# Kernel tuning notes

Measured on AMD Instinct MI355X. Metric: run time of the kernel, lower is better.

## Reference

```python
import jax, jax.numpy as jnp
import numpy as np

E = 1024  # embed_dim
H = 16    # num_heads
D = E // H  # head_dim


def setup_inputs() -> dict:
    key = jax.random.key(0)
    ks = jax.random.split(key, 9)
    s = 0.02
    return {
        "hidden_state": jax.random.normal(ks[0], (4, 1024, E), jnp.float32),
        "Wq": jax.random.normal(ks[1], (H, D, E), jnp.float32) * s,
        "bq": jax.random.normal(ks[2], (H, D), jnp.float32) * s,
        "Wk": jax.random.normal(ks[3], (H, D, E), jnp.float32) * s,
        "bk": jax.random.normal(ks[4], (H, D), jnp.float32) * s,
        "Wv": jax.random.normal(ks[5], (H, D, E), jnp.float32) * s,
        "bv": jax.random.normal(ks[6], (H, D), jnp.float32) * s,
        "Wo": jax.random.normal(ks[7], (E, E), jnp.float32) * s,
        "bo": jax.random.normal(ks[8], (E,), jnp.float32) * s,
    }


def _mha(x, Wq, bq, Wk, bk, Wv, bv, Wo, bo):
    # Per-head linear projections (torch Linear: y = x W^T + b), batched over heads.
    q = jnp.einsum("bse,hde->bhsd", x, Wq) + bq[None, :, None, :]
    k = jnp.einsum("bse,hde->bhsd", x, Wk) + bk[None, :, None, :]
    v = jnp.einsum("bse,hde->bhsd", x, Wv) + bv[None, :, None, :]
    scores = jnp.einsum("bhsd,bhtd->bhst", q, k) / jnp.sqrt(jnp.asarray(D, x.dtype))
    w = jax.nn.softmax(scores, axis=-1)  # F.softmax default -> last dim
    o = jnp.einsum("bhst,bhtd->bhsd", w, v)
    # concat heads along last dim: [B,S,H*D] in head order (matches torch.cat)
    B, _, S, _ = o.shape
    o = jnp.transpose(o, (0, 2, 1, 3)).reshape(B, S, H * D)
    return o @ Wo.T + bo


def reference(hidden_state, Wq, bq, Wk, bk, Wv, bv, Wo, bo):
    return _mha(hidden_state, Wq, bq, Wk, bk, Wv, bv, Wo, bo)
```

## Files before the change

### kernel.cpp

```cpp
#include <hip/hip_runtime.h>
#include <hip/hip_bf16.h>
#include <stdint.h>

#define E_DIM 1024
#define H_NUM 16
#define D_DIM 64
#define B_NUM 4
#define S_LEN 1024

typedef __attribute__((ext_vector_type(8))) short bf16x8;
typedef __attribute__((ext_vector_type(4))) short bf16x4;
typedef __attribute__((ext_vector_type(4))) float f32x4;

#define SOFTMAX_C2 0.18033688011112042f

__device__ inline ushort f2b(float x) {
    __hip_bfloat16 h = __float2bfloat16(x);
    return *(ushort*)&h;
}
__device__ inline float b2f(ushort u) {
    __hip_bfloat16 h = *(__hip_bfloat16*)&u;
    return __bfloat162float(h);
}
__device__ inline uint pk2(float a, float b) {
    __hip_bfloat162 h = __float22bfloat162_rn(make_float2(a, b));
    return *(uint*)&h;
}

__device__ inline void gld16(const ushort* g, ushort* l) {
    __builtin_amdgcn_global_load_lds((const __attribute__((address_space(1))) void*)g,
                                     (__attribute__((address_space(3))) void*)l, 16, 0, 0);
}

__global__ __launch_bounds__(256)
void convert_all(const float* __restrict__ X,  const float* __restrict__ Wq,
                 const float* __restrict__ Wk, const float* __restrict__ Wv,
                 const float* __restrict__ Wo,
                 ushort* __restrict__ Xb, ushort* __restrict__ Wcat,
                 ushort* __restrict__ Wob)
{
    const int bid = blockIdx.x;
    const float* src; ushort* dst; size_t off;
    if (bid < 4096)      { src = X;  dst = Xb;   off = (size_t)bid * 1024; }
    else if (bid < 5120) { src = Wq; dst = Wcat;              off = (size_t)(bid - 4096) * 1024; }
    else if (bid < 6144) { src = Wk; dst = Wcat + (1u << 20); off = (size_t)(bid - 5120) * 1024; }
    else if (bid < 7168) { src = Wv; dst = Wcat + (2u << 20); off = (size_t)(bid - 6144) * 1024; }
    else                 { src = Wo; dst = Wob;               off = (size_t)(bid - 7168) * 1024; }
    const size_t i = off + (size_t)threadIdx.x * 4;
    float4 v = *(const float4*)&src[i];
    ushort4 o;
    o.x = f2b(v.x); o.y = f2b(v.y); o.z = f2b(v.z); o.w = f2b(v.w);
    *(ushort4*)&dst[i] = o;
}

__global__ __launch_bounds__(256, 3)
void gemm_qkv(const ushort* __restrict__ A, const ushort* __restrict__ Bw,
              const float* __restrict__ b0, const float* __restrict__ b1,
              const float* __restrict__ b2,
              ushort* __restrict__ Qb, ushort* __restrict__ Kb,
              ushort* __restrict__ Vt_g, int K)
{
    __shared__ __align__(16) ushort SM[24576];
    ushort* As = SM;
    ushort* Bs = SM + 16384;

    const int tid  = threadIdx.x;
    const int wave = tid >> 6;
    const int lane = tid & 63;
    const int quad = lane >> 4;
    const int l16  = lane & 15;
    const int wm   = wave & 1;
    const int wn   = wave >> 1;
    const int m0   = blockIdx.x * 128;
    const int n0   = blockIdx.y * 64;

    f32x4 acc[4][2] = {};

    auto stageA = [&](int buf, int k0) {
#pragma unroll
        for (int i = 0; i < 4; ++i) {
            const int e   = i * 256 + tid;
            const int row = e >> 3;
            const int gc8 = ((e & 7) ^ (row & 7)) * 8;
            gld16(&A[(size_t)(m0 + row) * K + k0 + gc8], &As[buf * 8192 + e * 8]);
        }
    };
    auto stageB = [&](int buf, int k0) {
#pragma unroll
        for (int i = 0; i < 2; ++i) {
            const int e   = i * 256 + tid;
            const int row = e >> 3;
            const int gc8 = ((e & 7) ^ (row & 7)) * 8;
            gld16(&Bw[(size_t)(n0 + row) * K + k0 + gc8], &Bs[buf * 4096 + e * 8]);
        }
    };

    stageA(0, 0); stageB(0, 0);
    __syncthreads();

    const int nk = K >> 6;
    const int xa = (l16 & 7) * 8;
    for (int ki = 0; ki < nk; ++ki) {
        const int cur = ki & 1;
        if (ki + 1 < nk) { stageA(cur ^ 1, (ki + 1) << 6); stageB(cur ^ 1, (ki + 1) << 6); }

#pragma unroll
        for (int ks = 0; ks < 2; ++ks) {
            const int lc = (ks * 32 + quad * 8) ^ xa;
            bf16x8 af[4], bf[2];
#pragma unroll
            for (int mi = 0; mi < 4; ++mi)
                af[mi] = *(const bf16x8*)&As[cur * 8192 + (wm * 64 + mi * 16 + l16) * 64 + lc];
#pragma unroll
            for (int ni = 0; ni < 2; ++ni)
                bf[ni] = *(const bf16x8*)&Bs[cur * 4096 + (wn * 32 + ni * 16 + l16) * 64 + lc];
#pragma unroll
            for (int mi = 0; mi < 4; ++mi)
#pragma unroll
                for (int ni = 0; ni < 2; ++ni)
                    acc[mi][ni] = __builtin_amdgcn_mfma_f32_16x16x32_bf16(af[mi], bf[ni], acc[mi][ni], 0, 0, 0);
        }
        __syncthreads();
    }

    const int seg   = n0 >> 10;
    const int cbase = n0 & 1023;
    const float* bp = (seg == 0) ? b0 : (seg == 1) ? b1 : b2;
    const float scl = (seg == 0) ? SOFTMAX_C2 : 1.0f;

    if (seg < 2) {
        ushort* T = SM;
#pragma unroll
        for (int ni = 0; ni < 2; ++ni) {
            const int nloc = wn * 32 + ni * 16 + l16;
            const float bv = bp[cbase + nloc];
#pragma unroll
            for (int mi = 0; mi < 4; ++mi)
#pragma unroll
                for (int r = 0; r < 4; ++r)
                    T[(wm * 64 + mi * 16 + quad * 4 + r) * 72 + nloc] =
                        f2b((acc[mi][ni][r] + bv) * scl);
        }
        __syncthreads();
        ushort* dst = (seg == 0) ? Qb : Kb;
        const int row = tid >> 1, half = tid & 1;
        const ushort* s = &T[row * 72 + half * 32];
        ushort* d = &dst[(size_t)(m0 + row) * 1024 + cbase + half * 32];
#pragma unroll
        for (int j = 0; j < 4; ++j)
            *(uint4*)(d + j * 8) = *(const uint4*)(s + j * 8);
    } else {
        ushort* Tt = SM;
        const int hh = cbase >> 6;
        const int b  = m0 >> 10, sbase = m0 & 1023;
#pragma unroll
        for (int ni = 0; ni < 2; ++ni) {
            const int nloc = wn * 32 + ni * 16 + l16;
            const float bv = bp[cbase + nloc];
#pragma unroll
            for (int mi = 0; mi < 4; ++mi) {
                const int mloc = wm * 64 + mi * 16 + quad * 4;
                ushort4 pk;
                pk.x = f2b(acc[mi][ni][0] + bv);
                pk.y = f2b(acc[mi][ni][1] + bv);
                pk.z = f2b(acc[mi][ni][2] + bv);
                pk.w = f2b(acc[mi][ni][3] + bv);
                *(ushort4*)&Tt[nloc * 136 + mloc] = pk;
            }
        }
        __syncthreads();
        const int nrow = tid >> 2, qtr = tid & 3;
        const ushort* s = &Tt[nrow * 136 + qtr * 32];
        ushort* d = &Vt_g[(((size_t)(b * 16 + hh)) * 64 + nrow) * 1024 + sbase + qtr * 32];
#pragma unroll
        for (int j = 0; j < 4; ++j)
            *(uint4*)(d + j * 8) = *(const uint4*)(s + j * 8);
    }
}

__global__ __launch_bounds__(256, 8)
void attention7(const ushort* __restrict__ Qg, const ushort* __restrict__ Kg,
                const ushort* __restrict__ Vg,
                ushort* __restrict__ Opart, float* __restrict__ Lpart)
{
    __shared__ __align__(16) ushort SM[9216];

    const int tid  = threadIdx.x;
    const int w    = tid >> 6;
    const int lane = tid & 63;
    const int quad = lane >> 4;
    const int l16  = lane & 15;

    const int gid = blockIdx.x;
    const int qt  = (gid >> 3) & 15;
    const int grp = (gid & 7) | ((gid >> 7) << 3);
    const int bh  = grp & 63;
    const int th  = grp >> 6;
    const int b   = bh >> 4;
    const int h   = bh & 15;
    const size_t tbase = ((size_t)b * S_LEN) * E_DIM + (size_t)h * D_DIM;
    const size_t vbase = (size_t)bh * D_DIM * S_LEN;
    const int t0 = th * 512;

    const ushort* qrow = Qg + tbase + (size_t)(qt * 64 + w * 16 + l16) * E_DIM + quad * 8;
    bf16x8 qf[2];
    qf[0] = *(const bf16x8*)qrow;
    qf[1] = *(const bf16x8*)(qrow + 32);

    const int krow = tid >> 3, kslot = tid & 7;
    const int vr   = tid >> 2, vc = (tid & 3) * 8;

    auto stageK = [&](int buf, int tg) {
        gld16(&Kg[tbase + (size_t)(tg + krow) * E_DIM + ((kslot ^ (krow & 7)) * 8)],
              &SM[buf * 2048 + tid * 8]);
    };

    stageK(0, t0);
    {
        uint4 v0 = *(const uint4*)&Vg[vbase + (size_t)vr * S_LEN + t0 + vc];
        *(uint4*)&SM[4096 + vr * 40 + vc] = v0;
    }
    __syncthreads();

    float lq = 0.0f;
    f32x4 oacc[4] = {};
    const int xk = (l16 & 7);

    for (int kt = 0; kt < 16; ++kt) {
        const int cur = kt & 1;

        uint4 vpre;
        if (kt < 15) {
            const int tg = t0 + (kt + 1) * 32;
            stageK(cur ^ 1, tg);
            vpre = *(const uint4*)&Vg[vbase + (size_t)vr * S_LEN + tg + vc];
        }

        f32x4 sacc[2] = {};
#pragma unroll
        for (int mt = 0; mt < 2; ++mt)
#pragma unroll
            for (int ks = 0; ks < 2; ++ks) {
                bf16x8 kf = *(const bf16x8*)&SM[cur * 2048 + (mt * 16 + l16) * 64 +
                                                (((ks * 4 + quad) ^ xk) * 8)];
                sacc[mt] = __builtin_amdgcn_mfma_f32_16x16x32_bf16(kf, qf[ks], sacc[mt], 0, 0, 0);
            }

        bf16x4 pf[2];
        float rs = 0.0f;
#pragma unroll
        for (int mt = 0; mt < 2; ++mt) {
            float p0 = exp2f(sacc[mt][0]);
            float p1 = exp2f(sacc[mt][1]);
            float p2 = exp2f(sacc[mt][2]);
            float p3 = exp2f(sacc[mt][3]);
            rs += (p0 + p1) + (p2 + p3);
            union { uint uu[2]; bf16x4 v; } pk;
            pk.uu[0] = pk2(p0, p1);
            pk.uu[1] = pk2(p2, p3);
            pf[mt] = pk.v;
        }
        lq += rs;

#pragma unroll
        for (int nb = 0; nb < 4; ++nb)
#pragma unroll
            for (int kb = 0; kb < 2; ++kb) {
                bf16x4 vf = *(const bf16x4*)&SM[4096 + cur * 2560 +
                                                (nb * 16 + l16) * 40 + kb * 16 + quad * 4];
                oacc[nb] = __builtin_amdgcn_mfma_f32_16x16x16bf16_1k(pf[kb], vf, oacc[nb], 0, 0, 0);
            }

        if (kt < 15)
            *(uint4*)&SM[4096 + (cur ^ 1) * 2560 + vr * 40 + vc] = vpre;
        __syncthreads();
    }

    lq += __shfl_xor(lq, 16);
    lq += __shfl_xor(lq, 32);
    const size_t obase = ((size_t)(th * 64 + bh)) * S_LEN;
    if (lane < 16)
        Lpart[obase + qt * 64 + w * 16 + l16] = lq;

    ushort* T = SM;
#pragma unroll
    for (int nb = 0; nb < 4; ++nb)
#pragma unroll
        for (int r = 0; r < 4; ++r)
            T[(w * 16 + quad * 4 + r) * 72 + nb * 16 + l16] = f2b(oacc[nb][r]);
    __syncthreads();
    {
        const int row = tid >> 2, c16 = (tid & 3) * 16;
        const ushort* s = &T[row * 72 + c16];
        ushort* d = &Opart[(obase + qt * 64 + row) * 64 + c16];
        *(uint4*)(d)     = *(const uint4*)(s);
        *(uint4*)(d + 8) = *(const uint4*)(s + 8);
    }
}

__global__ __launch_bounds__(256, 4)
void gemm_out(const ushort* __restrict__ Opart, const float* __restrict__ Lpart,
              const ushort* __restrict__ Bw, const float* __restrict__ bias,
              float* __restrict__ Cout)
{
    __shared__ __align__(16) ushort SM[17408];
    ushort* As = SM;
    ushort* Bs = SM + 9216;

    const int tid  = threadIdx.x;
    const int w    = tid >> 6;
    const int lane = tid & 63;
    const int quad = lane >> 4;
    const int l16  = lane & 15;
    const int m0   = blockIdx.x * 64;
    const int n0   = blockIdx.y * 64;

    const int arow = tid >> 2;
    const int acol = (tid & 3) * 16;
    const int m    = m0 + arow;
    const int ab   = m >> 10;
    const int as   = m & 1023;

    f32x4 acc[4] = {};

    auto loadA = [&](int ki, uint4* o0, uint4* o1, float* linv) {
        const int bh = ab * 16 + ki;
        const size_t p0 = ((size_t)bh * 1024 + as) * 64 + acol;
        const size_t p1 = ((size_t)(64 + bh) * 1024 + as) * 64 + acol;
#pragma unroll
        for (int j = 0; j < 2; ++j) {
            o0[j] = *(const uint4*)&Opart[p0 + j * 8];
            o1[j] = *(const uint4*)&Opart[p1 + j * 8];
        }
        const float l0 = Lpart[(size_t)bh * 1024 + as];
        const float l1 = Lpart[(size_t)(64 + bh) * 1024 + as];
        *linv = 1.0f / (l0 + l1);
    };
    auto writeA = [&](int buf, const uint4* o0, const uint4* o1, float linv) {
        ushort* dst = &As[buf * 4608 + arow * 72 + acol];
#pragma unroll
        for (int j = 0; j < 2; ++j) {
            const ushort* a = (const ushort*)&o0[j];
            const ushort* c = (const ushort*)&o1[j];
            union { uint uu[4]; uint4 v; } pk;
            pk.uu[0] = pk2((b2f(a[0]) + b2f(c[0])) * linv, (b2f(a[1]) + b2f(c[1])) * linv);
            pk.uu[1] = pk2((b2f(a[2]) + b2f(c[2])) * linv, (b2f(a[3]) + b2f(c[3])) * linv);
            pk.uu[2] = pk2((b2f(a[4]) + b2f(c[4])) * linv, (b2f(a[5]) + b2f(c[5])) * linv);
            pk.uu[3] = pk2((b2f(a[6]) + b2f(c[6])) * linv, (b2f(a[7]) + b2f(c[7])) * linv);
            *(uint4*)(dst + j * 8) = pk.v;
        }
    };
    auto stageB = [&](int buf, int k0) {
#pragma unroll
        for (int i = 0; i < 2; ++i) {
            const int e   = i * 256 + tid;
            const int row = e >> 3;
            const int gc8 = ((e & 7) ^ (row & 7)) * 8;
            gld16(&Bw[(size_t)(n0 + row) * 1024 + k0 + gc8], &Bs[buf * 4096 + e * 8]);
        }
    };

    {
        uint4 o0[2], o1[2]; float linv;
        loadA(0, o0, o1, &linv);
        writeA(0, o0, o1, linv);
        stageB(0, 0);
    }
    __syncthreads();

    const int xa = (l16 & 7) * 8;
    for (int ki = 0; ki < 16; ++ki) {
        const int cur = ki & 1;

        uint4 o0[2], o1[2]; float linv;
        if (ki + 1 < 16) {
            loadA(ki + 1, o0, o1, &linv);
            stageB(cur ^ 1, (ki + 1) << 6);
        }

#pragma unroll
        for (int ks = 0; ks < 2; ++ks) {
            bf16x8 af = *(const bf16x8*)&As[cur * 4608 + (w * 16 + l16) * 72 + ks * 32 + quad * 8];
#pragma unroll
            for (int nb = 0; nb < 4; ++nb) {
                const int lcB = (ks * 32 + quad * 8) ^ xa;
                bf16x8 bf = *(const bf16x8*)&Bs[cur * 4096 + (nb * 16 + l16) * 64 + lcB];
                acc[nb] = __builtin_amdgcn_mfma_f32_16x16x32_bf16(af, bf, acc[nb], 0, 0, 0);
            }
        }

        if (ki + 1 < 16) writeA(cur ^ 1, o0, o1, linv);
        __syncthreads();
    }

    float* Tf = (float*)SM;
#pragma unroll
    for (int nb = 0; nb < 4; ++nb) {
        const float bv = bias[n0 + nb * 16 + l16];
#pragma unroll
        for (int r = 0; r < 4; ++r)
            Tf[(w * 16 + quad * 4 + r) * 68 + nb * 16 + l16] = acc[nb][r] + bv;
    }
    __syncthreads();
    {
        const int row = tid >> 2, c16 = (tid & 3) * 16;
        const float* s = &Tf[row * 68 + c16];
        float* d = &Cout[(size_t)(m0 + row) * 1024 + n0 + c16];
#pragma unroll
        for (int j = 0; j < 4; ++j)
            *(float4*)(d + j * 4) = *(const float4*)(s + j * 4);
    }
}

extern "C" void kernel_launch(void* const* d_in, const int* in_sizes, int n_in,
                              void* d_out, int out_size, void* d_ws, size_t ws_size,
                              hipStream_t stream)
{
    (void)in_sizes; (void)n_in; (void)out_size; (void)ws_size;

    const float* X  = (const float*)d_in[0];
    const float* Wq = (const float*)d_in[1];
    const float* bq = (const float*)d_in[2];
    const float* Wk = (const float*)d_in[3];
    const float* bk = (const float*)d_in[4];
    const float* Wv = (const float*)d_in[5];
    const float* bv = (const float*)d_in[6];
    const float* Wo = (const float*)d_in[7];
    const float* bo = (const float*)d_in[8];

    const size_t MEG = 1u << 20;
    ushort* ws    = (ushort*)d_ws;
    ushort* Xb    = ws;
    ushort* Wcat  = ws + 4 * MEG;
    ushort* Wob   = ws + 7 * MEG;
    ushort* Qb    = ws + 8 * MEG;
    ushort* Kb    = ws + 12 * MEG;
    ushort* Vtg   = ws + 16 * MEG;
    ushort* Opart = ws + 20 * MEG;
    float*  Lpart = (float*)(ws + 28 * MEG);

    dim3 blk(256);

    convert_all<<<8192, blk, 0, stream>>>(X, Wq, Wk, Wv, Wo, Xb, Wcat, Wob);

    gemm_qkv<<<dim3(32, 48), blk, 0, stream>>>(Xb, Wcat, bq, bk, bv,
                                               Qb, Kb, Vtg, E_DIM);

    attention7<<<2048, blk, 0, stream>>>(Qb, Kb, Vtg, Opart, Lpart);

    gemm_out<<<dim3(64, 16), blk, 0, stream>>>(Opart, Lpart, Wob, bo,
                                               (float*)d_out);
}
```

Before: 188.5 us.

## Process two query sub-tiles per warp to reuse K/V fragments

Each attention block now covers 128 query rows instead of 64, with every wave handling two 16-row sub-tiles. Each K and V fragment loaded from shared memory then feeds two MFMAs, which halves LDS and global K/V traffic per query row and halves the grid to 1024 blocks. The V staging row pitch also changes from 40 to 36 elements. In exchange, register pressure roughly doubles for accumulators, launch bounds drop to 4 blocks per CU, and the smaller grid gives fewer blocks to spread across CUs.

```diff
diff --git a/kernel.cpp b/kernel.cpp
--- a/kernel.cpp
+++ b/kernel.cpp
@@ -178,8 +178,8 @@
     }
 }
 
-__global__ __launch_bounds__(256, 8)
-void attention7(const ushort* __restrict__ Qg, const ushort* __restrict__ Kg,
+__global__ __launch_bounds__(256, 4)
+void attention8(const ushort* __restrict__ Qg, const ushort* __restrict__ Kg,
                 const ushort* __restrict__ Vg,
                 ushort* __restrict__ Opart, float* __restrict__ Lpart)
 {
@@ -192,8 +192,8 @@
     const int l16  = lane & 15;
 
     const int gid = blockIdx.x;
-    const int qt  = (gid >> 3) & 15;
-    const int grp = (gid & 7) | ((gid >> 7) << 3);
+    const int qt  = (gid >> 3) & 7;
+    const int grp = (gid & 7) | ((gid >> 6) << 3);
     const int bh  = grp & 63;
     const int th  = grp >> 6;
     const int b   = bh >> 4;
@@ -202,10 +202,14 @@
     const size_t vbase = (size_t)bh * D_DIM * S_LEN;
     const int t0 = th * 512;
 
-    const ushort* qrow = Qg + tbase + (size_t)(qt * 64 + w * 16 + l16) * E_DIM + quad * 8;
-    bf16x8 qf[2];
-    qf[0] = *(const bf16x8*)qrow;
-    qf[1] = *(const bf16x8*)(qrow + 32);
+    bf16x8 qf[2][2];
+#pragma unroll
+    for (int i = 0; i < 2; ++i) {
+        const ushort* qrow = Qg + tbase +
+            (size_t)(qt * 128 + w * 32 + i * 16 + l16) * E_DIM + quad * 8;
+        qf[i][0] = *(const bf16x8*)qrow;
+        qf[i][1] = *(const bf16x8*)(qrow + 32);
+    }
 
     const int krow = tid >> 3, kslot = tid & 7;
     const int vr   = tid >> 2, vc = (tid & 3) * 8;
@@ -218,12 +222,12 @@
     stageK(0, t0);
     {
         uint4 v0 = *(const uint4*)&Vg[vbase + (size_t)vr * S_LEN + t0 + vc];
-        *(uint4*)&SM[4096 + vr * 40 + vc] = v0;
+        *(uint4*)&SM[4096 + vr * 36 + vc] = v0;
     }
     __syncthreads();
 
-    float lq = 0.0f;
-    f32x4 oacc[4] = {};
+    float lq[2] = {0.0f, 0.0f};
+    f32x4 oacc[2][4] = {};
     const int xk = (l16 & 7);
 
     for (int kt = 0; kt < 16; ++kt) {
@@ -236,65 +240,83 @@
             vpre = *(const uint4*)&Vg[vbase + (size_t)vr * S_LEN + tg + vc];
         }
 
-        f32x4 sacc[2] = {};
+        f32x4 sacc[2][2] = {};
 #pragma unroll
         for (int mt = 0; mt < 2; ++mt)
 #pragma unroll
             for (int ks = 0; ks < 2; ++ks) {
                 bf16x8 kf = *(const bf16x8*)&SM[cur * 2048 + (mt * 16 + l16) * 64 +
                                                 (((ks * 4 + quad) ^ xk) * 8)];
-                sacc[mt] = __builtin_amdgcn_mfma_f32_16x16x32_bf16(kf, qf[ks], sacc[mt], 0, 0, 0);
+#pragma unroll
+                for (int i = 0; i < 2; ++i)
+                    sacc[i][mt] = __builtin_amdgcn_mfma_f32_16x16x32_bf16(
+                        kf, qf[i][ks], sacc[i][mt], 0, 0, 0);
             }
 
-        bf16x4 pf[2];
-        float rs = 0.0f;
-#pragma unroll
-        for (int mt = 0; mt < 2; ++mt) {
-            float p0 = exp2f(sacc[mt][0]);
-            float p1 = exp2f(sacc[mt][1]);
-            float p2 = exp2f(sacc[mt][2]);
-            float p3 = exp2f(sacc[mt][3]);
-            rs += (p0 + p1) + (p2 + p3);
-            union { uint uu[2]; bf16x4 v; } pk;
-            pk.uu[0] = pk2(p0, p1);
-            pk.uu[1] = pk2(p2, p3);
-            pf[mt] = pk.v;
-        }
-        lq += rs;
+        bf16x4 pf[2][2];
+#pragma unroll
+        for (int i = 0; i < 2; ++i) {
+            float rs = 0.0f;
+#pragma unroll
+            for (int mt = 0; mt < 2; ++mt) {
+                float p0 = exp2f(sacc[i][mt][0]);
+                float p1 = exp2f(sacc[i][mt][1]);
+                float p2 = exp2f(sacc[i][mt][2]);
+                float p3 = exp2f(sacc[i][mt][3]);
+                rs += (p0 + p1) + (p2 + p3);
+                union { uint uu[2]; bf16x4 v; } pk;
+                pk.uu[0] = pk2(p0, p1);
+                pk.uu[1] = pk2(p2, p3);
+                pf[i][mt] = pk.v;
+            }
+            lq[i] += rs;
+        }
 
 #pragma unroll
         for (int nb = 0; nb < 4; ++nb)
 #pragma unroll
             for (int kb = 0; kb < 2; ++kb) {
-                bf16x4 vf = *(const bf16x4*)&SM[4096 + cur * 2560 +
-                                                (nb * 16 + l16) * 40 + kb * 16 + quad * 4];
-                oacc[nb] = __builtin_amdgcn_mfma_f32_16x16x16bf16_1k(pf[kb], vf, oacc[nb], 0, 0, 0);
+                bf16x4 vf = *(const bf16x4*)&SM[4096 + cur * 2304 +
+                                                (nb * 16 + l16) * 36 + kb * 16 + quad * 4];
+#pragma unroll
+                for (int i = 0; i < 2; ++i)
+                    oacc[i][nb] = __builtin_amdgcn_mfma_f32_16x16x16bf16_1k(
+                        pf[i][kb], vf, oacc[i][nb], 0, 0, 0);
             }
 
         if (kt < 15)
-            *(uint4*)&SM[4096 + (cur ^ 1) * 2560 + vr * 40 + vc] = vpre;
+            *(uint4*)&SM[4096 + (cur ^ 1) * 2304 + vr * 36 + vc] = vpre;
         __syncthreads();
     }
 
-    lq += __shfl_xor(lq, 16);
-    lq += __shfl_xor(lq, 32);
     const size_t obase = ((size_t)(th * 64 + bh)) * S_LEN;
-    if (lane < 16)
-        Lpart[obase + qt * 64 + w * 16 + l16] = lq;
+#pragma unroll
+    for (int i = 0; i < 2; ++i) {
+        lq[i] += __shfl_xor(lq[i], 16);
+        lq[i] += __shfl_xor(lq[i], 32);
+    }
+    if (lane < 16) {
+        Lpart[obase + qt * 128 + w * 32 + l16]      = lq[0];
+        Lpart[obase + qt * 128 + w * 32 + 16 + l16] = lq[1];
+    }
 
     ushort* T = SM;
 #pragma unroll
-    for (int nb = 0; nb < 4; ++nb)
-#pragma unroll
-        for (int r = 0; r < 4; ++r)
-            T[(w * 16 + quad * 4 + r) * 72 + nb * 16 + l16] = f2b(oacc[nb][r]);
+    for (int i = 0; i < 2; ++i)
+#pragma unroll
+        for (int nb = 0; nb < 4; ++nb)
+#pragma unroll
+            for (int r = 0; r < 4; ++r)
+                T[(w * 32 + i * 16 + quad * 4 + r) * 72 + nb * 16 + l16] =
+                    f2b(oacc[i][nb][r]);
     __syncthreads();
     {
-        const int row = tid >> 2, c16 = (tid & 3) * 16;
-        const ushort* s = &T[row * 72 + c16];
-        ushort* d = &Opart[(obase + qt * 64 + row) * 64 + c16];
-        *(uint4*)(d)     = *(const uint4*)(s);
-        *(uint4*)(d + 8) = *(const uint4*)(s + 8);
+        const int row = tid >> 1, half = tid & 1;
+        const ushort* s = &T[row * 72 + half * 32];
+        ushort* d = &Opart[(obase + qt * 128 + row) * 64 + half * 32];
+#pragma unroll
+        for (int j = 0; j < 4; ++j)
+            *(uint4*)(d + j * 8) = *(const uint4*)(s + j * 8);
     }
 }
 
@@ -446,7 +468,7 @@
     gemm_qkv<<<dim3(32, 48), blk, 0, stream>>>(Xb, Wcat, bq, bk, bv,
                                                Qb, Kb, Vtg, E_DIM);
 
-    attention7<<<2048, blk, 0, stream>>>(Qb, Kb, Vtg, Opart, Lpart);
+    attention8<<<1024, blk, 0, stream>>>(Qb, Kb, Vtg, Opart, Lpart);
 
     gemm_out<<<dim3(64, 16), blk, 0, stream>>>(Opart, Lpart, Wob, bo,
                                                (float*)d_out);
```

Result: no change. 186.8 us (-0.9%).

## Drop key-split in attention, normalize in-kernel, and stream normalized output to GEMM

Applied to the files above, without the earlier changes.

Attention no longer splits the key range into two halves with partial outputs and row sums. Each block now processes all 1024 keys, normalizes by the reciprocal row sum, and writes bf16 output directly in [B,S,E] layout. The output projection can then stage A straight into LDS with async global-to-LDS copies, dropping the combine/rescale step and the partial-sum buffers. This halves the attention grid to 1024 blocks, each with a longer loop, which lowers parallelism. It also swaps exp2f for the raw hardware exp2 intrinsic and shrinks the V tile padding.

```diff
diff --git a/kernel.cpp b/kernel.cpp
--- a/kernel.cpp
+++ b/kernel.cpp
@@ -26,6 +26,7 @@
     __hip_bfloat162 h = __float22bfloat162_rn(make_float2(a, b));
     return *(uint*)&h;
 }
+__device__ inline float fexp2(float x) { return __builtin_amdgcn_exp2f(x); }
 
 __device__ inline void gld16(const ushort* g, ushort* l) {
     __builtin_amdgcn_global_load_lds((const __attribute__((address_space(1))) void*)g,
@@ -179,9 +180,8 @@
 }
 
 __global__ __launch_bounds__(256, 8)
-void attention7(const ushort* __restrict__ Qg, const ushort* __restrict__ Kg,
-                const ushort* __restrict__ Vg,
-                ushort* __restrict__ Opart, float* __restrict__ Lpart)
+void attention11(const ushort* __restrict__ Qg, const ushort* __restrict__ Kg,
+                 const ushort* __restrict__ Vg, ushort* __restrict__ Anorm)
 {
     __shared__ __align__(16) ushort SM[9216];
 
@@ -193,14 +193,11 @@
 
     const int gid = blockIdx.x;
     const int qt  = (gid >> 3) & 15;
-    const int grp = (gid & 7) | ((gid >> 7) << 3);
-    const int bh  = grp & 63;
-    const int th  = grp >> 6;
+    const int bh  = (gid & 7) | ((gid >> 7) << 3);
     const int b   = bh >> 4;
     const int h   = bh & 15;
     const size_t tbase = ((size_t)b * S_LEN) * E_DIM + (size_t)h * D_DIM;
     const size_t vbase = (size_t)bh * D_DIM * S_LEN;
-    const int t0 = th * 512;
 
     const ushort* qrow = Qg + tbase + (size_t)(qt * 64 + w * 16 + l16) * E_DIM + quad * 8;
     bf16x8 qf[2];
@@ -210,15 +207,13 @@
     const int krow = tid >> 3, kslot = tid & 7;
     const int vr   = tid >> 2, vc = (tid & 3) * 8;
 
-    auto stageK = [&](int buf, int tg) {
-        gld16(&Kg[tbase + (size_t)(tg + krow) * E_DIM + ((kslot ^ (krow & 7)) * 8)],
-              &SM[buf * 2048 + tid * 8]);
-    };
-
-    stageK(0, t0);
+    const ushort* kptr = Kg + tbase + (size_t)krow * E_DIM + ((kslot ^ (krow & 7)) * 8);
+    const ushort* vptr = Vg + vbase + (size_t)vr * S_LEN + vc;
+
+    gld16(kptr, &SM[tid * 8]);
     {
-        uint4 v0 = *(const uint4*)&Vg[vbase + (size_t)vr * S_LEN + t0 + vc];
-        *(uint4*)&SM[4096 + vr * 40 + vc] = v0;
+        uint4 v0 = *(const uint4*)vptr;
+        *(uint4*)&SM[4096 + vr * 36 + vc] = v0;
     }
     __syncthreads();
 
@@ -226,14 +221,15 @@
     f32x4 oacc[4] = {};
     const int xk = (l16 & 7);
 
-    for (int kt = 0; kt < 16; ++kt) {
+    for (int kt = 0; kt < 32; ++kt) {
         const int cur = kt & 1;
 
         uint4 vpre;
-        if (kt < 15) {
-            const int tg = t0 + (kt + 1) * 32;
-            stageK(cur ^ 1, tg);
-            vpre = *(const uint4*)&Vg[vbase + (size_t)vr * S_LEN + tg + vc];
+        if (kt < 31) {
+            kptr += 32 * E_DIM;
+            gld16(kptr, &SM[(cur ^ 1) * 2048 + tid * 8]);
+            vptr += 32;
+            vpre = *(const uint4*)vptr;
         }
 
         f32x4 sacc[2] = {};
@@ -250,10 +246,10 @@
         float rs = 0.0f;
 #pragma unroll
         for (int mt = 0; mt < 2; ++mt) {
-            float p0 = exp2f(sacc[mt][0]);
-            float p1 = exp2f(sacc[mt][1]);
-            float p2 = exp2f(sacc[mt][2]);
-            float p3 = exp2f(sacc[mt][3]);
+            float p0 = fexp2(sacc[mt][0]);
+            float p1 = fexp2(sacc[mt][1]);
+            float p2 = fexp2(sacc[mt][2]);
+            float p3 = fexp2(sacc[mt][3]);
             rs += (p0 + p1) + (p2 + p3);
             union { uint uu[2]; bf16x4 v; } pk;
             pk.uu[0] = pk2(p0, p1);
@@ -266,46 +262,47 @@
         for (int nb = 0; nb < 4; ++nb)
 #pragma unroll
             for (int kb = 0; kb < 2; ++kb) {
-                bf16x4 vf = *(const bf16x4*)&SM[4096 + cur * 2560 +
-                                                (nb * 16 + l16) * 40 + kb * 16 + quad * 4];
+                bf16x4 vf = *(const bf16x4*)&SM[4096 + cur * 2304 +
+                                                (nb * 16 + l16) * 36 + kb * 16 + quad * 4];
                 oacc[nb] = __builtin_amdgcn_mfma_f32_16x16x16bf16_1k(pf[kb], vf, oacc[nb], 0, 0, 0);
             }
 
-        if (kt < 15)
-            *(uint4*)&SM[4096 + (cur ^ 1) * 2560 + vr * 40 + vc] = vpre;
+        if (kt < 31)
+            *(uint4*)&SM[4096 + (cur ^ 1) * 2304 + vr * 36 + vc] = vpre;
         __syncthreads();
     }
 
     lq += __shfl_xor(lq, 16);
     lq += __shfl_xor(lq, 32);
-    const size_t obase = ((size_t)(th * 64 + bh)) * S_LEN;
-    if (lane < 16)
-        Lpart[obase + qt * 64 + w * 16 + l16] = lq;
+
+    float linv[4];
+#pragma unroll
+    for (int r = 0; r < 4; ++r)
+        linv[r] = __builtin_amdgcn_rcpf(__shfl(lq, quad * 4 + r));
 
     ushort* T = SM;
 #pragma unroll
     for (int nb = 0; nb < 4; ++nb)
 #pragma unroll
         for (int r = 0; r < 4; ++r)
-            T[(w * 16 + quad * 4 + r) * 72 + nb * 16 + l16] = f2b(oacc[nb][r]);
+            T[(w * 16 + quad * 4 + r) * 72 + nb * 16 + l16] = f2b(oacc[nb][r] * linv[r]);
     __syncthreads();
     {
         const int row = tid >> 2, c16 = (tid & 3) * 16;
         const ushort* s = &T[row * 72 + c16];
-        ushort* d = &Opart[(obase + qt * 64 + row) * 64 + c16];
+        ushort* d = &Anorm[(size_t)(b * 1024 + qt * 64 + row) * 1024 + h * 64 + c16];
         *(uint4*)(d)     = *(const uint4*)(s);
         *(uint4*)(d + 8) = *(const uint4*)(s + 8);
     }
 }
 
 __global__ __launch_bounds__(256, 4)
-void gemm_out(const ushort* __restrict__ Opart, const float* __restrict__ Lpart,
-              const ushort* __restrict__ Bw, const float* __restrict__ bias,
-              float* __restrict__ Cout)
+void gemm_out(const ushort* __restrict__ A, const ushort* __restrict__ Bw,
+              const float* __restrict__ bias, float* __restrict__ Cout)
 {
-    __shared__ __align__(16) ushort SM[17408];
+    __shared__ __align__(16) ushort SM[16384];
     ushort* As = SM;
-    ushort* Bs = SM + 9216;
+    ushort* Bs = SM + 8192;
 
     const int tid  = threadIdx.x;
     const int w    = tid >> 6;
@@ -315,39 +312,15 @@
     const int m0   = blockIdx.x * 64;
     const int n0   = blockIdx.y * 64;
 
-    const int arow = tid >> 2;
-    const int acol = (tid & 3) * 16;
-    const int m    = m0 + arow;
-    const int ab   = m >> 10;
-    const int as   = m & 1023;
-
     f32x4 acc[4] = {};
 
-    auto loadA = [&](int ki, uint4* o0, uint4* o1, float* linv) {
-        const int bh = ab * 16 + ki;
-        const size_t p0 = ((size_t)bh * 1024 + as) * 64 + acol;
-        const size_t p1 = ((size_t)(64 + bh) * 1024 + as) * 64 + acol;
-#pragma unroll
-        for (int j = 0; j < 2; ++j) {
-            o0[j] = *(const uint4*)&Opart[p0 + j * 8];
-            o1[j] = *(const uint4*)&Opart[p1 + j * 8];
-        }
-        const float l0 = Lpart[(size_t)bh * 1024 + as];
-        const float l1 = Lpart[(size_t)(64 + bh) * 1024 + as];
-        *linv = 1.0f / (l0 + l1);
-    };
-    auto writeA = [&](int buf, const uint4* o0, const uint4* o1, float linv) {
-        ushort* dst = &As[buf * 4608 + arow * 72 + acol];
-#pragma unroll
-        for (int j = 0; j < 2; ++j) {
-            const ushort* a = (const ushort*)&o0[j];
-            const ushort* c = (const ushort*)&o1[j];
-            union { uint uu[4]; uint4 v; } pk;
-            pk.uu[0] = pk2((b2f(a[0]) + b2f(c[0])) * linv, (b2f(a[1]) + b2f(c[1])) * linv);
-            pk.uu[1] = pk2((b2f(a[2]) + b2f(c[2])) * linv, (b2f(a[3]) + b2f(c[3])) * linv);
-            pk.uu[2] = pk2((b2f(a[4]) + b2f(c[4])) * linv, (b2f(a[5]) + b2f(c[5])) * linv);
-            pk.uu[3] = pk2((b2f(a[6]) + b2f(c[6])) * linv, (b2f(a[7]) + b2f(c[7])) * linv);
-            *(uint4*)(dst + j * 8) = pk.v;
+    auto stageA = [&](int buf, int k0) {
+#pragma unroll
+        for (int i = 0; i < 2; ++i) {
+            const int e   = i * 256 + tid;
+            const int row = e >> 3;
+            const int gc8 = ((e & 7) ^ (row & 7)) * 8;
+            gld16(&A[(size_t)(m0 + row) * 1024 + k0 + gc8], &As[buf * 4096 + e * 8]);
         }
     };
     auto stageB = [&](int buf, int k0) {
@@ -360,36 +333,24 @@
         }
     };
 
-    {
-        uint4 o0[2], o1[2]; float linv;
-        loadA(0, o0, o1, &linv);
-        writeA(0, o0, o1, linv);
-        stageB(0, 0);
-    }
+    stageA(0, 0); stageB(0, 0);
     __syncthreads();
 
     const int xa = (l16 & 7) * 8;
     for (int ki = 0; ki < 16; ++ki) {
         const int cur = ki & 1;
-
-        uint4 o0[2], o1[2]; float linv;
-        if (ki + 1 < 16) {
-            loadA(ki + 1, o0, o1, &linv);
-            stageB(cur ^ 1, (ki + 1) << 6);
-        }
+        if (ki + 1 < 16) { stageA(cur ^ 1, (ki + 1) << 6); stageB(cur ^ 1, (ki + 1) << 6); }
 
 #pragma unroll
         for (int ks = 0; ks < 2; ++ks) {
-            bf16x8 af = *(const bf16x8*)&As[cur * 4608 + (w * 16 + l16) * 72 + ks * 32 + quad * 8];
+            const int lc = (ks * 32 + quad * 8) ^ xa;
+            bf16x8 af = *(const bf16x8*)&As[cur * 4096 + (w * 16 + l16) * 64 + lc];
 #pragma unroll
             for (int nb = 0; nb < 4; ++nb) {
-                const int lcB = (ks * 32 + quad * 8) ^ xa;
-                bf16x8 bf = *(const bf16x8*)&Bs[cur * 4096 + (nb * 16 + l16) * 64 + lcB];
+                bf16x8 bf = *(const bf16x8*)&Bs[cur * 4096 + (nb * 16 + l16) * 64 + lc];
                 acc[nb] = __builtin_amdgcn_mfma_f32_16x16x32_bf16(af, bf, acc[nb], 0, 0, 0);
             }
         }
-
-        if (ki + 1 < 16) writeA(cur ^ 1, o0, o1, linv);
         __syncthreads();
     }
 
@@ -436,8 +397,7 @@
     ushort* Qb    = ws + 8 * MEG;
     ushort* Kb    = ws + 12 * MEG;
     ushort* Vtg   = ws + 16 * MEG;
-    ushort* Opart = ws + 20 * MEG;
-    float*  Lpart = (float*)(ws + 28 * MEG);
+    ushort* Anorm = ws + 20 * MEG;
 
     dim3 blk(256);
 
@@ -446,8 +406,7 @@
     gemm_qkv<<<dim3(32, 48), blk, 0, stream>>>(Xb, Wcat, bq, bk, bv,
                                                Qb, Kb, Vtg, E_DIM);
 
-    attention7<<<2048, blk, 0, stream>>>(Qb, Kb, Vtg, Opart, Lpart);
-
-    gemm_out<<<dim3(64, 16), blk, 0, stream>>>(Opart, Lpart, Wob, bo,
-                                               (float*)d_out);
-}
+    attention11<<<1024, blk, 0, stream>>>(Qb, Kb, Vtg, Anorm);
+
+    gemm_out<<<dim3(64, 16), blk, 0, stream>>>(Anorm, Wob, bo, (float*)d_out);
+}
```

Result: faster. 176.0 us (-6.7%).
